# Kernel optimization log

Measured on AMD Instinct MI355X. Metric: run time of the kernel, lower is better.

The kernel has to match this reference:

```python
import jax, jax.numpy as jnp
import numpy as np

HIDDEN = 32
INPUT = 1
OUTPUT = 1


def setup_inputs() -> dict:
    key = jax.random.key(0)
    ks = jax.random.split(key, 7)
    B, T = 4096, 512
    s_ih = 1.0 / np.sqrt(HIDDEN)
    x = jax.random.normal(ks[0], (B, T, INPUT), dtype=jnp.float32)
    # PyTorch LSTM params, gate order i, f, g, o
    W_ih = jax.random.uniform(ks[1], (4 * HIDDEN, INPUT), jnp.float32, -s_ih, s_ih)
    W_hh = jax.random.uniform(ks[2], (4 * HIDDEN, HIDDEN), jnp.float32, -s_ih, s_ih)
    b_ih = jax.random.uniform(ks[3], (4 * HIDDEN,), jnp.float32, -s_ih, s_ih)
    b_hh = jax.random.uniform(ks[4], (4 * HIDDEN,), jnp.float32, -s_ih, s_ih)
    W_fc = jax.random.uniform(ks[5], (OUTPUT, HIDDEN), jnp.float32, -s_ih, s_ih)
    b_fc = jax.random.uniform(ks[6], (OUTPUT,), jnp.float32, -s_ih, s_ih)
    return {"x": x, "W_ih": W_ih, "W_hh": W_hh, "b_ih": b_ih,
            "b_hh": b_hh, "W_fc": W_fc, "b_fc": b_fc}


def _lstm_last_h(x, W_ih, W_hh, b_ih, b_hh):
    B = x.shape[0]
    H = W_hh.shape[1]
    # precompute input contribution for all timesteps: [T, B, 4H]
    xg = jnp.einsum('bti,gi->tbg', x, W_ih) + (b_ih + b_hh)

    def step(carry, xg_t):
        h, c = carry
        gates = xg_t + h @ W_hh.T  # [B, 4H]
        i, f, g, o = jnp.split(gates, 4, axis=-1)
        i = jax.nn.sigmoid(i)
        f = jax.nn.sigmoid(f)
        g = jnp.tanh(g)
        o = jax.nn.sigmoid(o)
        c = f * c + i * g
        h = o * jnp.tanh(c)
        return (h, c), None

    h0 = jnp.zeros((B, H), x.dtype)
    c0 = jnp.zeros((B, H), x.dtype)
    (hT, _), _ = jax.lax.scan(step, (h0, c0), xg)
    return hT  # last timestep hidden state [B, H]


def reference(x, W_ih, W_hh, b_ih, b_hh, W_fc, b_fc):
    hT = _lstm_last_h(x, W_ih, W_hh, b_ih, b_hh)
    return hT @ W_fc.T + b_fc  # [B, OUTPUT]
```

## Files before the change

kernel.cpp:

```cpp
#include <hip/hip_runtime.h>


#define HID 32
#define TSTEPS 512
#define BPW 2
#define BLOCK 64
#define L2E 1.44269504088896340736f

__device__ __forceinline__ float rcp_fast(float x) {
    return __builtin_amdgcn_rcpf(x);
}
__device__ __forceinline__ float exp2_fast(float x) {
    return __builtin_amdgcn_exp2f(x);
}
__device__ __forceinline__ float sigmoid_l2(float a) {
    return rcp_fast(1.0f + exp2_fast(-a));
}
__device__ __forceinline__ float tanh_l2(float a) {
    return fmaf(2.0f, rcp_fast(1.0f + exp2_fast(-a)), -1.0f);
}

__global__ __launch_bounds__(BLOCK)
__attribute__((amdgpu_waves_per_eu(2, 2)))
void lstm_fused_kernel(const float* __restrict__ x,
                       const float* __restrict__ W_ih,
                       const float* __restrict__ W_hh,
                       const float* __restrict__ b_ih,
                       const float* __restrict__ b_hh,
                       const float* __restrict__ W_fc,
                       const float* __restrict__ b_fc,
                       float* __restrict__ out)
{
    __shared__ __align__(16) float x_s[BPW * TSTEPS];
    __shared__ __align__(16) float h_s[BPW][HID];

    const int tid = threadIdx.x;
    const int lb  = tid >> 5;
    const int j   = tid & 31;
    const int b0  = blockIdx.x * BPW;

    {
        const float4* xsrc = reinterpret_cast<const float4*>(x + (size_t)b0 * TSTEPS);
        float4* xdst = reinterpret_cast<float4*>(x_s);
        #pragma unroll
        for (int k = 0; k < (BPW * TSTEPS) / (4 * BLOCK); ++k)
            xdst[tid + k * BLOCK] = xsrc[tid + k * BLOCK];
    }

    float w0[HID], w1[HID], w2[HID], w3[HID];
    {
        const float4* r0 = reinterpret_cast<const float4*>(W_hh + (size_t)(0 * HID + j) * HID);
        const float4* r1 = reinterpret_cast<const float4*>(W_hh + (size_t)(1 * HID + j) * HID);
        const float4* r2 = reinterpret_cast<const float4*>(W_hh + (size_t)(2 * HID + j) * HID);
        const float4* r3 = reinterpret_cast<const float4*>(W_hh + (size_t)(3 * HID + j) * HID);
        #pragma unroll
        for (int k = 0; k < HID / 4; ++k) {
            float4 v;
            v = r0[k]; w0[4*k]=v.x*L2E;      w0[4*k+1]=v.y*L2E;      w0[4*k+2]=v.z*L2E;      w0[4*k+3]=v.w*L2E;
            v = r1[k]; w1[4*k]=v.x*L2E;      w1[4*k+1]=v.y*L2E;      w1[4*k+2]=v.z*L2E;      w1[4*k+3]=v.w*L2E;
            v = r2[k]; w2[4*k]=v.x*2.0f*L2E; w2[4*k+1]=v.y*2.0f*L2E; w2[4*k+2]=v.z*2.0f*L2E; w2[4*k+3]=v.w*2.0f*L2E;
            v = r3[k]; w3[4*k]=v.x*L2E;      w3[4*k+1]=v.y*L2E;      w3[4*k+2]=v.z*L2E;      w3[4*k+3]=v.w*L2E;
        }
    }
    const float wih0 = W_ih[j]         * L2E;
    const float wih1 = W_ih[HID + j]   * L2E;
    const float wih2 = W_ih[2*HID + j] * 2.0f * L2E;
    const float wih3 = W_ih[3*HID + j] * L2E;
    const float bs0  = (b_ih[j]         + b_hh[j])         * L2E;
    const float bs1  = (b_ih[HID + j]   + b_hh[HID + j])   * L2E;
    const float bs2  = (b_ih[2*HID + j] + b_hh[2*HID + j]) * 2.0f * L2E;
    const float bs3  = (b_ih[3*HID + j] + b_hh[3*HID + j]) * L2E;

    h_s[lb][j] = 0.0f;
    float c = 0.0f, hcur = 0.0f;

    #pragma unroll 1
    for (int t = 0; t < TSTEPS; ++t) {
        const float xv = x_s[lb * TSTEPS + t];

        float a0 = fmaf(xv, wih0, bs0);
        float a1 = fmaf(xv, wih1, bs1);
        float a2 = fmaf(xv, wih2, bs2);
        float a3 = fmaf(xv, wih3, bs3);

        const float4* hr = reinterpret_cast<const float4*>(&h_s[lb][0]);
        #pragma unroll
        for (int k = 0; k < HID / 4; ++k) {
            float4 hv = hr[k];
            a0 = fmaf(hv.x, w0[4*k  ], a0);
            a1 = fmaf(hv.x, w1[4*k  ], a1);
            a2 = fmaf(hv.x, w2[4*k  ], a2);
            a3 = fmaf(hv.x, w3[4*k  ], a3);
            a0 = fmaf(hv.y, w0[4*k+1], a0);
            a1 = fmaf(hv.y, w1[4*k+1], a1);
            a2 = fmaf(hv.y, w2[4*k+1], a2);
            a3 = fmaf(hv.y, w3[4*k+1], a3);
            a0 = fmaf(hv.z, w0[4*k+2], a0);
            a1 = fmaf(hv.z, w1[4*k+2], a1);
            a2 = fmaf(hv.z, w2[4*k+2], a2);
            a3 = fmaf(hv.z, w3[4*k+2], a3);
            a0 = fmaf(hv.w, w0[4*k+3], a0);
            a1 = fmaf(hv.w, w1[4*k+3], a1);
            a2 = fmaf(hv.w, w2[4*k+3], a2);
            a3 = fmaf(hv.w, w3[4*k+3], a3);
        }

        const float ig = sigmoid_l2(a0);
        const float fg = sigmoid_l2(a1);
        const float gg = tanh_l2(a2);
        const float og = sigmoid_l2(a3);
        c    = fmaf(fg, c, ig * gg);
        hcur = og * tanh_l2((2.0f * L2E) * c);

        h_s[lb][j] = hcur;
    }

    float p = hcur * W_fc[j];
    #pragma unroll
    for (int off = 16; off >= 1; off >>= 1)
        p += __shfl_xor(p, off);
    if (j == 0)
        out[b0 + lb] = p + b_fc[0];
}

extern "C" void kernel_launch(void* const* d_in, const int* in_sizes, int n_in,
                              void* d_out, int out_size, void* d_ws, size_t ws_size,
                              hipStream_t stream) {
    const float* x    = (const float*)d_in[0];
    const float* W_ih = (const float*)d_in[1];
    const float* W_hh = (const float*)d_in[2];
    const float* b_ih = (const float*)d_in[3];
    const float* b_hh = (const float*)d_in[4];
    const float* W_fc = (const float*)d_in[5];
    const float* b_fc = (const float*)d_in[6];
    float* out = (float*)d_out;

    const int B = in_sizes[0] / TSTEPS;
    const int grid = B / BPW;
    lstm_fused_kernel<<<grid, BLOCK, 0, stream>>>(x, W_ih, W_hh, b_ih, b_hh,
                                                  W_fc, b_fc, out);
}
```

Measured before the change: 281.4 us.

## Split LSTM gates across wave halves, one batch row per block

After: 300.1 us. +6.6%, slower.

```diff
diff --git a/kernel.cpp b/kernel.cpp
--- a/kernel.cpp
+++ b/kernel.cpp
@@ -3,9 +3,10 @@
 
 #define HID 32
 #define TSTEPS 512
-#define BPW 2
 #define BLOCK 64
 #define L2E 1.44269504088896340736f
+
+#define OPAQUE(v) asm("" : "+v"(v))
 
 __device__ __forceinline__ float rcp_fast(float x) {
     return __builtin_amdgcn_rcpf(x);
@@ -13,15 +14,9 @@
 __device__ __forceinline__ float exp2_fast(float x) {
     return __builtin_amdgcn_exp2f(x);
 }
-__device__ __forceinline__ float sigmoid_l2(float a) {
-    return rcp_fast(1.0f + exp2_fast(-a));
-}
-__device__ __forceinline__ float tanh_l2(float a) {
-    return fmaf(2.0f, rcp_fast(1.0f + exp2_fast(-a)), -1.0f);
-}
 
 __global__ __launch_bounds__(BLOCK)
-__attribute__((amdgpu_waves_per_eu(2, 2)))
+__attribute__((amdgpu_waves_per_eu(4, 4)))
 void lstm_fused_kernel(const float* __restrict__ x,
                        const float* __restrict__ W_ih,
                        const float* __restrict__ W_hh,
@@ -31,96 +26,96 @@
                        const float* __restrict__ b_fc,
                        float* __restrict__ out)
 {
-    __shared__ __align__(16) float x_s[BPW * TSTEPS];
-    __shared__ __align__(16) float h_s[BPW][HID];
+    __shared__ __align__(16) float x_s[TSTEPS];
+    __shared__ __align__(16) float h_s[HID];
 
     const int tid = threadIdx.x;
-    const int lb  = tid >> 5;
     const int j   = tid & 31;
-    const int b0  = blockIdx.x * BPW;
+    const int hi  = tid >> 5;
+    const int b   = blockIdx.x;
 
     {
-        const float4* xsrc = reinterpret_cast<const float4*>(x + (size_t)b0 * TSTEPS);
+        const float4* xsrc = reinterpret_cast<const float4*>(x + (size_t)b * TSTEPS);
         float4* xdst = reinterpret_cast<float4*>(x_s);
-        #pragma unroll
-        for (int k = 0; k < (BPW * TSTEPS) / (4 * BLOCK); ++k)
-            xdst[tid + k * BLOCK] = xsrc[tid + k * BLOCK];
+        xdst[tid]      = xsrc[tid];
+        xdst[tid + 64] = xsrc[tid + 64];
     }
 
-    float w0[HID], w1[HID], w2[HID], w3[HID];
+    const int rowA = hi * HID + j;
+    const int rowB = 2 * HID + hi * HID + j;
+
+    float wA[HID], wB[HID];
     {
-        const float4* r0 = reinterpret_cast<const float4*>(W_hh + (size_t)(0 * HID + j) * HID);
-        const float4* r1 = reinterpret_cast<const float4*>(W_hh + (size_t)(1 * HID + j) * HID);
-        const float4* r2 = reinterpret_cast<const float4*>(W_hh + (size_t)(2 * HID + j) * HID);
-        const float4* r3 = reinterpret_cast<const float4*>(W_hh + (size_t)(3 * HID + j) * HID);
+        const float4* rA = reinterpret_cast<const float4*>(W_hh + (size_t)rowA * HID);
+        const float4* rB = reinterpret_cast<const float4*>(W_hh + (size_t)rowB * HID);
         #pragma unroll
         for (int k = 0; k < HID / 4; ++k) {
             float4 v;
-            v = r0[k]; w0[4*k]=v.x*L2E;      w0[4*k+1]=v.y*L2E;      w0[4*k+2]=v.z*L2E;      w0[4*k+3]=v.w*L2E;
-            v = r1[k]; w1[4*k]=v.x*L2E;      w1[4*k+1]=v.y*L2E;      w1[4*k+2]=v.z*L2E;      w1[4*k+3]=v.w*L2E;
-            v = r2[k]; w2[4*k]=v.x*2.0f*L2E; w2[4*k+1]=v.y*2.0f*L2E; w2[4*k+2]=v.z*2.0f*L2E; w2[4*k+3]=v.w*2.0f*L2E;
-            v = r3[k]; w3[4*k]=v.x*L2E;      w3[4*k+1]=v.y*L2E;      w3[4*k+2]=v.z*L2E;      w3[4*k+3]=v.w*L2E;
+            v = rA[k]; wA[4*k]=v.x; wA[4*k+1]=v.y; wA[4*k+2]=v.z; wA[4*k+3]=v.w;
+            v = rB[k]; wB[4*k]=v.x; wB[4*k+1]=v.y; wB[4*k+2]=v.z; wB[4*k+3]=v.w;
         }
+        #pragma unroll
+        for (int m = 0; m < HID; ++m) { OPAQUE(wA[m]); OPAQUE(wB[m]); }
     }
-    const float wih0 = W_ih[j]         * L2E;
-    const float wih1 = W_ih[HID + j]   * L2E;
-    const float wih2 = W_ih[2*HID + j] * 2.0f * L2E;
-    const float wih3 = W_ih[3*HID + j] * L2E;
-    const float bs0  = (b_ih[j]         + b_hh[j])         * L2E;
-    const float bs1  = (b_ih[HID + j]   + b_hh[HID + j])   * L2E;
-    const float bs2  = (b_ih[2*HID + j] + b_hh[2*HID + j]) * 2.0f * L2E;
-    const float bs3  = (b_ih[3*HID + j] + b_hh[3*HID + j]) * L2E;
+    const float wihA = W_ih[rowA];
+    const float wihB = W_ih[rowB];
+    const float bsA  = b_ih[rowA] + b_hh[rowA];
+    const float bsB  = b_ih[rowB] + b_hh[rowB];
 
-    h_s[lb][j] = 0.0f;
+    const float sA = -L2E;
+    const float sB = hi ? -L2E : -2.0f * L2E;
+    const float mB = hi ? 1.0f : 2.0f;
+    const float aB = hi ? 0.0f : -1.0f;
+
+    h_s[j] = 0.0f;
     float c = 0.0f, hcur = 0.0f;
 
     #pragma unroll 1
     for (int t = 0; t < TSTEPS; ++t) {
-        const float xv = x_s[lb * TSTEPS + t];
+        const float xv = x_s[t];
 
-        float a0 = fmaf(xv, wih0, bs0);
-        float a1 = fmaf(xv, wih1, bs1);
-        float a2 = fmaf(xv, wih2, bs2);
-        float a3 = fmaf(xv, wih3, bs3);
+        float GA = fmaf(xv, wihA, bsA);
+        float GB = fmaf(xv, wihB, bsB);
 
-        const float4* hr = reinterpret_cast<const float4*>(&h_s[lb][0]);
+        const float4* hr = reinterpret_cast<const float4*>(h_s);
         #pragma unroll
         for (int k = 0; k < HID / 4; ++k) {
             float4 hv = hr[k];
-            a0 = fmaf(hv.x, w0[4*k  ], a0);
-            a1 = fmaf(hv.x, w1[4*k  ], a1);
-            a2 = fmaf(hv.x, w2[4*k  ], a2);
-            a3 = fmaf(hv.x, w3[4*k  ], a3);
-            a0 = fmaf(hv.y, w0[4*k+1], a0);
-            a1 = fmaf(hv.y, w1[4*k+1], a1);
-            a2 = fmaf(hv.y, w2[4*k+1], a2);
-            a3 = fmaf(hv.y, w3[4*k+1], a3);
-            a0 = fmaf(hv.z, w0[4*k+2], a0);
-            a1 = fmaf(hv.z, w1[4*k+2], a1);
-            a2 = fmaf(hv.z, w2[4*k+2], a2);
-            a3 = fmaf(hv.z, w3[4*k+2], a3);
-            a0 = fmaf(hv.w, w0[4*k+3], a0);
-            a1 = fmaf(hv.w, w1[4*k+3], a1);
-            a2 = fmaf(hv.w, w2[4*k+3], a2);
-            a3 = fmaf(hv.w, w3[4*k+3], a3);
+            GA = fmaf(hv.x, wA[4*k  ], GA);
+            GB = fmaf(hv.x, wB[4*k  ], GB);
+            GA = fmaf(hv.y, wA[4*k+1], GA);
+            GB = fmaf(hv.y, wB[4*k+1], GB);
+            GA = fmaf(hv.z, wA[4*k+2], GA);
+            GB = fmaf(hv.z, wB[4*k+2], GB);
+            GA = fmaf(hv.w, wA[4*k+3], GA);
+            GB = fmaf(hv.w, wB[4*k+3], GB);
         }
 
-        const float ig = sigmoid_l2(a0);
-        const float fg = sigmoid_l2(a1);
-        const float gg = tanh_l2(a2);
-        const float og = sigmoid_l2(a3);
-        c    = fmaf(fg, c, ig * gg);
-        hcur = og * tanh_l2((2.0f * L2E) * c);
+        const float actA = rcp_fast(1.0f + exp2_fast(GA * sA));
+        const float rB_  = rcp_fast(1.0f + exp2_fast(GB * sB));
+        const float resB = fmaf(mB, rB_, aB);
 
-        h_s[lb][j] = hcur;
+        const float s1 = __shfl_xor(actA, 32);
+        const float s2 = __shfl_xor(resB, 32);
+        const float ii = hi ? s1   : actA;
+        const float ff = hi ? actA : s1;
+        const float gg = hi ? s2   : resB;
+        const float oo = hi ? resB : s2;
+
+        c = fmaf(ff, c, ii * gg);
+        const float rC = rcp_fast(1.0f + exp2_fast(c * (-2.0f * L2E)));
+        const float tc = fmaf(2.0f, rC, -1.0f);
+        hcur = oo * tc;
+
+        h_s[j] = hcur;
     }
 
     float p = hcur * W_fc[j];
     #pragma unroll
     for (int off = 16; off >= 1; off >>= 1)
         p += __shfl_xor(p, off);
-    if (j == 0)
-        out[b0 + lb] = p + b_fc[0];
+    if (tid == 0)
+        out[b] = p + b_fc[0];
 }
 
 extern "C" void kernel_launch(void* const* d_in, const int* in_sizes, int n_in,
@@ -136,7 +131,6 @@
     float* out = (float*)d_out;
 
     const int B = in_sizes[0] / TSTEPS;
-    const int grid = B / BPW;
-    lstm_fused_kernel<<<grid, BLOCK, 0, stream>>>(x, W_ih, W_hh, b_ih, b_hh,
-                                                  W_fc, b_fc, out);
+    lstm_fused_kernel<<<B, BLOCK, 0, stream>>>(x, W_ih, W_hh, b_ih, b_hh,
+                                               W_fc, b_fc, out);
 }
```
